# Kernel optimization log

Measured on AMD Instinct MI355X. Metric: run time of the kernel, lower is better.

Reference implementation:

```python
import jax, jax.numpy as jnp
import numpy as np

B, N, C, T = 2048, 512, 64, 128  # batch, codebook size, latent channels, latent time


def setup_inputs() -> dict:
    key = jax.random.key(0)
    k1, k2 = jax.random.split(key)
    y = jax.random.normal(k1, (B, C, T), dtype=jnp.float32)   # encoder latents
    m = jax.random.normal(k2, (N, C, T), dtype=jnp.float32)   # centroid means
    sd = jnp.ones((N, C, T), dtype=jnp.float32)               # centroid variances
    p = jnp.zeros((N,), dtype=jnp.float32) + 1e-6             # cluster counts
    return {"y": y, "m": m, "sd": sd, "p": p}


def reference(y, m, sd, p):
    # --- squared-distance argmin assignment (same math as (y-m)^2 summed over C,T) ---
    b = y.shape[0]
    yf = y.reshape(b, -1)                 # [B, D]
    mf = m.reshape(m.shape[0], -1)        # [N, D]
    d2 = (yf * yf).sum(-1)[:, None] + (mf * mf).sum(-1)[None, :] - 2.0 * (yf @ mf.T)
    assign = jnp.argmin(d2, axis=1)       # [B] int assignments

    # --- sequential, order-sensitive EMA scatter updates (faithful to python loop) ---
    def step(carry, inp):
        p_, m_, sd_ = carry
        yi, zi = inp
        p_ = p_.at[zi].add(1.0)
        mi = m_[zi] * 0.001 + yi * 0.999
        m_ = m_.at[zi].set(mi)
        sdi = (mi - yi) ** 2 * 0.001 + sd_[zi] * 0.999
        sd_ = sd_.at[zi].set(sdi)
        return (p_, m_, sd_), None

    (p, m, sd), _ = jax.lax.scan(step, (p, m, sd), (y, assign))
    return m, sd, p, assign
```

## Files before the change

kernel.cpp:

```cpp
#include <hip/hip_runtime.h>
#include <hip/hip_bf16.h>


#define Bb 2048
#define Nn 512
#define Dd 8192
#define MARGIN 12.0f
#define KC 8
#define KSTEPS 32

typedef __attribute__((ext_vector_type(4))) float f32x4;
typedef __attribute__((ext_vector_type(8))) short s16x8;

union Frag { unsigned u[4]; s16x8 s; };

__device__ inline unsigned pack2(float lo, float hi) {
    return __builtin_amdgcn_perm(__float_as_uint(hi), __float_as_uint(lo), 0x07060302u);
}

__device__ inline void ema4(float4& mcv, float4& scv, const float4 yv) {
#define EMA_C(c) { mcv.c = mcv.c * 0.001f + yv.c * 0.999f; \
                   float d_ = mcv.c - yv.c;                 \
                   scv.c = d_ * d_ * 0.001f + scv.c * 0.999f; }
    EMA_C(x) EMA_C(y) EMA_C(z) EMA_C(w)
#undef EMA_C
}

__global__ __launch_bounds__(256) void m_norms(const float* __restrict__ M,
                                               float* __restrict__ mm) {
    int n = blockIdx.x, t = threadIdx.x;
    const float4* r = (const float4*)(M + (size_t)n * Dd);
    float s = 0.f;
#pragma unroll
    for (int u = 0; u < 8; u++) {
        float4 v = r[t + 256 * u];
        s += v.x * v.x + v.y * v.y + v.z * v.z + v.w * v.w;
    }
    __shared__ float red[256];
    red[t] = s;
    __syncthreads();
    for (int off = 128; off > 0; off >>= 1) {
        if (t < off) red[t] += red[t + off];
        __syncthreads();
    }
    if (t == 0) mm[n] = red[0];
}

__global__ __launch_bounds__(512, 4) void gemm_coarse(const float* __restrict__ Y,
                                                      const float* __restrict__ M,
                                                      float* __restrict__ part) {
    __shared__ __align__(16) float As[128 * 32];
    __shared__ __align__(16) float Bs[128 * 32];
    const int t = threadIdx.x;
    const int lane = t & 63;
    const int w = t >> 6;
    const int ct = blockIdx.x, rt = blockIdx.y, kc = blockIdx.z;

    const size_t ybase = (size_t)rt * 128 * Dd + (size_t)kc * (KSTEPS * 32);
    const size_t mbase = (size_t)ct * 128 * Dd + (size_t)kc * (KSTEPS * 32);

    int rowS[2], soff[2];
#pragma unroll
    for (int u = 0; u < 2; u++) {
        int flat = (w * 2 + u) * 64 + lane;
        int row = flat >> 3, seg = flat & 7;
        rowS[u] = row;
        soff[u] = (seg ^ (row & 7)) * 4;
    }

    const int wr0 = (w & 3) * 32, wc0 = (w >> 2) * 64;
    const int l15 = lane & 15, quad = lane >> 4;

    f32x4 acc[2][4];
#pragma unroll
    for (int i = 0; i < 2; i++)
#pragma unroll
        for (int j = 0; j < 4; j++) acc[i][j] = (f32x4)(0.0f);

    for (int step = 0; step < KSTEPS; step++) {
        const int kpos = step * 32;
#pragma unroll
        for (int u = 0; u < 2; u++) {
            const float* gA = Y + ybase + (size_t)rowS[u] * Dd + kpos + soff[u];
            const float* gB = M + mbase + (size_t)rowS[u] * Dd + kpos + soff[u];
            __builtin_amdgcn_global_load_lds(
                (const __attribute__((address_space(1))) void*)gA,
                (__attribute__((address_space(3))) void*)(As + (w * 2 + u) * 256), 16, 0, 0);
            __builtin_amdgcn_global_load_lds(
                (const __attribute__((address_space(1))) void*)gB,
                (__attribute__((address_space(3))) void*)(Bs + (w * 2 + u) * 256), 16, 0, 0);
        }
        __syncthreads();

        Frag fa[2], fb[4];
#pragma unroll
        for (int ta = 0; ta < 2; ta++) {
            int rowa = wr0 + ta * 16 + l15;
            const float* Ar = As + rowa * 32;
            int s0 = ((quad * 2) ^ (rowa & 7)) * 4;
            int s1 = ((quad * 2 + 1) ^ (rowa & 7)) * 4;
            f32x4 x0 = *(const f32x4*)(Ar + s0);
            f32x4 x1 = *(const f32x4*)(Ar + s1);
            fa[ta].u[0] = pack2(x0[0], x0[1]);
            fa[ta].u[1] = pack2(x0[2], x0[3]);
            fa[ta].u[2] = pack2(x1[0], x1[1]);
            fa[ta].u[3] = pack2(x1[2], x1[3]);
        }
#pragma unroll
        for (int tb = 0; tb < 4; tb++) {
            int rowb = wc0 + tb * 16 + l15;
            const float* Br = Bs + rowb * 32;
            int s0 = ((quad * 2) ^ (rowb & 7)) * 4;
            int s1 = ((quad * 2 + 1) ^ (rowb & 7)) * 4;
            f32x4 x0 = *(const f32x4*)(Br + s0);
            f32x4 x1 = *(const f32x4*)(Br + s1);
            fb[tb].u[0] = pack2(x0[0], x0[1]);
            fb[tb].u[1] = pack2(x0[2], x0[3]);
            fb[tb].u[2] = pack2(x1[0], x1[1]);
            fb[tb].u[3] = pack2(x1[2], x1[3]);
        }
#pragma unroll
        for (int i = 0; i < 2; i++)
#pragma unroll
            for (int j = 0; j < 4; j++)
                acc[i][j] = __builtin_amdgcn_mfma_f32_16x16x32_bf16(fa[i].s, fb[j].s, acc[i][j], 0, 0, 0);
        __syncthreads();
    }

    float* P = part + (size_t)kc * (Bb * Nn);
#pragma unroll
    for (int i = 0; i < 2; i++) {
        int rg = rt * 128 + wr0 + i * 16 + quad * 4;
#pragma unroll
        for (int j = 0; j < 4; j++) {
            int cg = ct * 128 + wc0 + j * 16 + l15;
#pragma unroll
            for (int r = 0; r < 4; r++)
                P[(size_t)(rg + r) * Nn + cg] = acc[i][j][r];
        }
    }
}

__global__ __launch_bounds__(256) void rescore(const float* __restrict__ Y,
                                               const float* __restrict__ M,
                                               const float* __restrict__ part,
                                               const float* __restrict__ mm,
                                               float* __restrict__ assignF) {
    __shared__ float redW[4];
    __shared__ int candList[Nn];
    __shared__ float candD2[Nn];
    __shared__ int candCnt;
    int b = blockIdx.x, t = threadIdx.x, lane = t & 63, w = t >> 6;
    if (t == 0) candCnt = 0;

    int c0 = t, c1 = t + 256;
    float dot0 = 0.f, dot1 = 0.f;
#pragma unroll
    for (int k = 0; k < KC; k++) {
        dot0 += part[(size_t)k * (Bb * Nn) + (size_t)b * Nn + c0];
        dot1 += part[(size_t)k * (Bb * Nn) + (size_t)b * Nn + c1];
    }
    float d0 = mm[c0] - 2.0f * dot0;
    float d1 = mm[c1] - 2.0f * dot1;

    float mn = fminf(d0, d1);
#pragma unroll
    for (int off = 32; off > 0; off >>= 1) mn = fminf(mn, __shfl_xor(mn, off));
    if (lane == 0) redW[w] = mn;
    __syncthreads();
    float thresh = fminf(fminf(redW[0], redW[1]), fminf(redW[2], redW[3])) + MARGIN;

    if (d0 <= thresh) candList[atomicAdd(&candCnt, 1)] = c0;
    if (d1 <= thresh) candList[atomicAdd(&candCnt, 1)] = c1;
    __syncthreads();
    int ncand = candCnt;

    if (ncand == 1) {
        if (t == 0) assignF[b] = (float)candList[0];
        return;
    }

    const float4* yr = (const float4*)(Y + (size_t)b * Dd);
    for (int j = w; j < ncand; j += 4) {
        int c = candList[j];
        const float4* mr = (const float4*)(M + (size_t)c * Dd);
        float p = 0.f;
#pragma unroll 8
        for (int u = 0; u < 32; u++) {
            float4 yv = yr[u * 64 + lane];
            float4 mv = mr[u * 64 + lane];
            p += yv.x * mv.x + yv.y * mv.y + yv.z * mv.z + yv.w * mv.w;
        }
#pragma unroll
        for (int off = 32; off > 0; off >>= 1) p += __shfl_xor(p, off);
        if (lane == 0) candD2[j] = mm[c] - 2.0f * p;
    }
    __syncthreads();

    if (t == 0) {
        float bestV = 3.4e38f;
        int bestI = 0x3fffffff;
        for (int j = 0; j < ncand; j++) {
            float d2e = candD2[j];
            int c = candList[j];
            if (d2e < bestV || (d2e == bestV && c < bestI)) { bestV = d2e; bestI = c; }
        }
        assignF[b] = (float)bestI;
    }
}

__global__ __launch_bounds__(256) void ema_scatter(const float* __restrict__ Y,
                                                   const float* __restrict__ M0,
                                                   const float* __restrict__ SD0,
                                                   const float* __restrict__ P0,
                                                   const float* __restrict__ assignF,
                                                   float* __restrict__ m_out,
                                                   float* __restrict__ sd_out,
                                                   float* __restrict__ p_out) {
    __shared__ int lst[Bb];
    __shared__ int cntSh;
    int n = blockIdx.x, s = blockIdx.y, t = threadIdx.x, lane = t & 63, w = t >> 6;

    if (w == 0) {
        int cnt = 0;
#pragma unroll
        for (int u = 0; u < 32; u++) {
            int zi = (int)assignF[u * 64 + lane];
            unsigned long long mask = __ballot(zi == n);
            if (zi == n) lst[cnt + (int)__popcll(mask & ((1ull << lane) - 1ull))] = u * 64 + lane;
            cnt += (int)__popcll(mask);
        }
        if (lane == 0) {
            cntSh = cnt;
            if (s == 0) p_out[n] = P0[n] + (float)cnt;
        }
    }
    __syncthreads();
    int cnt = cntSh;

    size_t off = (size_t)n * Dd + (size_t)s * 1024;
    float4 mc = *(const float4*)(M0 + off + 4 * t);
    float4 sc = *(const float4*)(SD0 + off + 4 * t);

    int j = 0;
    for (; j + 16 <= cnt; j += 16) {
        float4 yv[16];
#pragma unroll
        for (int q = 0; q < 16; q++)
            yv[q] = *(const float4*)(Y + (size_t)lst[j + q] * Dd + (size_t)s * 1024 + 4 * t);
#pragma unroll
        for (int q = 0; q < 16; q++) ema4(mc, sc, yv[q]);
    }
    for (; j < cnt; j++) {
        float4 yv = *(const float4*)(Y + (size_t)lst[j] * Dd + (size_t)s * 1024 + 4 * t);
        ema4(mc, sc, yv);
    }

    *(float4*)(m_out + off + 4 * t) = mc;
    *(float4*)(sd_out + off + 4 * t) = sc;
}

extern "C" void kernel_launch(void* const* d_in, const int* in_sizes, int n_in,
                              void* d_out, int out_size, void* d_ws, size_t ws_size,
                              hipStream_t stream) {
    const float* y  = (const float*)d_in[0];
    const float* m  = (const float*)d_in[1];
    const float* sd = (const float*)d_in[2];
    const float* p  = (const float*)d_in[3];

    float* out     = (float*)d_out;
    float* m_out   = out;
    float* sd_out  = out + 4194304;
    float* p_out   = out + 8388608;
    float* assignF = out + 8389120;
    float* part    = out;

    m_norms    <<<Nn, 256, 0, stream>>>(m, p_out);
    gemm_coarse<<<dim3(4, 16, KC), 512, 0, stream>>>(y, m, part);
    rescore    <<<Bb, 256, 0, stream>>>(y, m, part, p_out, assignF);
    ema_scatter<<<dim3(Nn, 8), 256, 0, stream>>>(y, m, sd, p, assignF, m_out, sd_out, p_out);
}
```

Baseline: 228.2 us.

## Double-buffer GEMM LDS tiles and batch tail loads in EMA scatter loop

```diff
diff --git a/kernel.cpp b/kernel.cpp
--- a/kernel.cpp
+++ b/kernel.cpp
@@ -49,8 +49,8 @@
 __global__ __launch_bounds__(512, 4) void gemm_coarse(const float* __restrict__ Y,
                                                       const float* __restrict__ M,
                                                       float* __restrict__ part) {
-    __shared__ __align__(16) float As[128 * 32];
-    __shared__ __align__(16) float Bs[128 * 32];
+    __shared__ __align__(16) float As[2][128 * 32];
+    __shared__ __align__(16) float Bs[2][128 * 32];
     const int t = threadIdx.x;
     const int lane = t & 63;
     const int w = t >> 6;
@@ -68,6 +68,21 @@
         soff[u] = (seg ^ (row & 7)) * 4;
     }
 
+#define STAGE(buf, kpos)                                                          \
+    {                                                                             \
+        _Pragma("unroll")                                                         \
+        for (int u = 0; u < 2; u++) {                                             \
+            const float* gA = Y + ybase + (size_t)rowS[u] * Dd + (kpos) + soff[u];\
+            const float* gB = M + mbase + (size_t)rowS[u] * Dd + (kpos) + soff[u];\
+            __builtin_amdgcn_global_load_lds(                                     \
+                (const __attribute__((address_space(1))) void*)gA,                \
+                (__attribute__((address_space(3))) void*)(As[buf] + (w * 2 + u) * 256), 16, 0, 0); \
+            __builtin_amdgcn_global_load_lds(                                     \
+                (const __attribute__((address_space(1))) void*)gB,                \
+                (__attribute__((address_space(3))) void*)(Bs[buf] + (w * 2 + u) * 256), 16, 0, 0); \
+        }                                                                         \
+    }
+
     const int wr0 = (w & 3) * 32, wc0 = (w >> 2) * 64;
     const int l15 = lane & 15, quad = lane >> 4;
 
@@ -77,26 +92,20 @@
 #pragma unroll
         for (int j = 0; j < 4; j++) acc[i][j] = (f32x4)(0.0f);
 
+    STAGE(0, 0);
+    __syncthreads();
+
     for (int step = 0; step < KSTEPS; step++) {
-        const int kpos = step * 32;
-#pragma unroll
-        for (int u = 0; u < 2; u++) {
-            const float* gA = Y + ybase + (size_t)rowS[u] * Dd + kpos + soff[u];
-            const float* gB = M + mbase + (size_t)rowS[u] * Dd + kpos + soff[u];
-            __builtin_amdgcn_global_load_lds(
-                (const __attribute__((address_space(1))) void*)gA,
-                (__attribute__((address_space(3))) void*)(As + (w * 2 + u) * 256), 16, 0, 0);
-            __builtin_amdgcn_global_load_lds(
-                (const __attribute__((address_space(1))) void*)gB,
-                (__attribute__((address_space(3))) void*)(Bs + (w * 2 + u) * 256), 16, 0, 0);
-        }
-        __syncthreads();
-
+        const int cur = step & 1;
+        if (step + 1 < KSTEPS) STAGE(cur ^ 1, (step + 1) * 32);
+
+        const float* Acur = As[cur];
+        const float* Bcur = Bs[cur];
         Frag fa[2], fb[4];
 #pragma unroll
         for (int ta = 0; ta < 2; ta++) {
             int rowa = wr0 + ta * 16 + l15;
-            const float* Ar = As + rowa * 32;
+            const float* Ar = Acur + rowa * 32;
             int s0 = ((quad * 2) ^ (rowa & 7)) * 4;
             int s1 = ((quad * 2 + 1) ^ (rowa & 7)) * 4;
             f32x4 x0 = *(const f32x4*)(Ar + s0);
@@ -109,7 +118,7 @@
 #pragma unroll
         for (int tb = 0; tb < 4; tb++) {
             int rowb = wc0 + tb * 16 + l15;
-            const float* Br = Bs + rowb * 32;
+            const float* Br = Bcur + rowb * 32;
             int s0 = ((quad * 2) ^ (rowb & 7)) * 4;
             int s1 = ((quad * 2 + 1) ^ (rowb & 7)) * 4;
             f32x4 x0 = *(const f32x4*)(Br + s0);
@@ -126,6 +135,7 @@
                 acc[i][j] = __builtin_amdgcn_mfma_f32_16x16x32_bf16(fa[i].s, fb[j].s, acc[i][j], 0, 0, 0);
         __syncthreads();
     }
+#undef STAGE
 
     float* P = part + (size_t)kc * (Bb * Nn);
 #pragma unroll
@@ -242,18 +252,17 @@
     float4 mc = *(const float4*)(M0 + off + 4 * t);
     float4 sc = *(const float4*)(SD0 + off + 4 * t);
 
-    int j = 0;
-    for (; j + 16 <= cnt; j += 16) {
+    for (int base = 0; base < cnt; base += 16) {
         float4 yv[16];
 #pragma unroll
+        for (int q = 0; q < 16; q++) {
+            int jj = base + q;
+            int idx = lst[jj < cnt ? jj : cnt - 1];
+            yv[q] = *(const float4*)(Y + (size_t)idx * Dd + (size_t)s * 1024 + 4 * t);
+        }
+#pragma unroll
         for (int q = 0; q < 16; q++)
-            yv[q] = *(const float4*)(Y + (size_t)lst[j + q] * Dd + (size_t)s * 1024 + 4 * t);
-#pragma unroll
-        for (int q = 0; q < 16; q++) ema4(mc, sc, yv[q]);
-    }
-    for (; j < cnt; j++) {
-        float4 yv = *(const float4*)(Y + (size_t)lst[j] * Dd + (size_t)s * 1024 + 4 * t);
-        ema4(mc, sc, yv);
+            if (base + q < cnt) ema4(mc, sc, yv[q]);
     }
 
     *(float4*)(m_out + off + 4 * t) = mc;
```

Result: no change. 229.6 us (+0.6%).
